# Kernel tuning notes

Measured on AMD Instinct MI355X. Metric: run time of the kernel, lower is better.

The kernel has to match this reference:

```python
import jax, jax.numpy as jnp
import numpy as np

FEAT_STRIDE = 16
PRE_NMS_TOP_N = 4000
POST_NMS_TOP_N = 300
NMS_THRESH = 0.7


def _whctrs(a):
    w = a[2] - a[0] + 1.0
    h = a[3] - a[1] + 1.0
    return w, h, a[0] + 0.5 * (w - 1.0), a[1] + 0.5 * (h - 1.0)

def _mkanchors(ws, hs, xc, yc):
    ws = ws[:, None]; hs = hs[:, None]
    return np.hstack([xc - 0.5 * (ws - 1), yc - 0.5 * (hs - 1), xc + 0.5 * (ws - 1), yc + 0.5 * (hs - 1)])

def _ratio_enum(anchor, ratios):
    w, h, xc, yc = _whctrs(anchor)
    size = w * h
    ws = np.round(np.sqrt(size / ratios))
    hs = np.round(ws * ratios)
    return _mkanchors(ws, hs, xc, yc)

def _scale_enum(anchor, scales):
    w, h, xc, yc = _whctrs(anchor)
    return _mkanchors(w * scales, h * scales, xc, yc)

def generate_anchors(base_size, ratios, scales):
    base = np.array([1.0, 1.0, base_size, base_size], dtype=np.float64) - 1.0
    ra = _ratio_enum(base, np.asarray(ratios, dtype=np.float64))
    return np.vstack([_scale_enum(ra[i], np.asarray(scales, dtype=np.float64)) for i in range(ra.shape[0])]).astype(np.float32)

# ---- NMS: sequential greedy suppression over score-sorted boxes ----

def _nms_keep(boxes, thresh):
    # boxes: [N,4] sorted by descending score. Legacy +1 area convention.
    boxes = jax.lax.stop_gradient(boxes)
    x1, y1, x2, y2 = boxes[:, 0], boxes[:, 1], boxes[:, 2], boxes[:, 3]
    areas = (x2 - x1 + 1.0) * (y2 - y1 + 1.0)
    xx1 = jnp.maximum(x1[:, None], x1[None, :])
    yy1 = jnp.maximum(y1[:, None], y1[None, :])
    xx2 = jnp.minimum(x2[:, None], x2[None, :])
    yy2 = jnp.minimum(y2[:, None], y2[None, :])
    w = jnp.maximum(xx2 - xx1 + 1.0, 0.0)
    h = jnp.maximum(yy2 - yy1 + 1.0, 0.0)
    inter = w * h
    iou = inter / (areas[:, None] + areas[None, :] - inter)
    sup = iou > thresh  # [N,N]
    n = boxes.shape[0]
    idxs = jnp.arange(n)

    def body(suppressed, i):
        kept = ~suppressed[i]
        suppressed = suppressed | (kept & sup[i] & (idxs > i))
        return suppressed, kept

    _, keep = jax.lax.scan(body, jnp.zeros((n,), dtype=bool), idxs)
    return keep  # [N] bool

# ---- forward ----

def _forward(scores, bbox_deltas, im_info, anchors):
    A = anchors.shape[0]
    B = bbox_deltas.shape[0]
    H, W = scores.shape[2], scores.shape[3]
    sc = scores[:, A:, :, :]  # fg scores [B,A,H,W]

    # anchor grid: K = H*W shifts, anchors broadcast over shifts (K major, A minor)
    shift_x = jnp.arange(W, dtype=scores.dtype) * FEAT_STRIDE
    shift_y = jnp.arange(H, dtype=scores.dtype) * FEAT_STRIDE
    sx, sy = jnp.meshgrid(shift_x, shift_y)  # 'xy' indexing, like np.meshgrid
    shifts = jnp.stack([sx.ravel(), sy.ravel(), sx.ravel(), sy.ravel()], axis=1)  # [K,4]
    all_anchors = (anchors[None, :, :] + shifts[:, None, :]).reshape(-1, 4)  # [K*A,4]

    deltas = bbox_deltas.transpose(0, 2, 3, 1).reshape(B, -1, 4)  # [B,N,4]
    scr = sc.transpose(0, 2, 3, 1).reshape(B, -1)  # [B,N]

    # bbox_transform_inv
    widths = all_anchors[:, 2] - all_anchors[:, 0] + 1.0
    heights = all_anchors[:, 3] - all_anchors[:, 1] + 1.0
    ctr_x = all_anchors[:, 0] + 0.5 * widths
    ctr_y = all_anchors[:, 1] + 0.5 * heights
    dx, dy, dw, dh = deltas[..., 0], deltas[..., 1], deltas[..., 2], deltas[..., 3]
    pcx = dx * widths + ctr_x
    pcy = dy * heights + ctr_y
    pw = jnp.exp(dw) * widths
    ph = jnp.exp(dh) * heights
    px1 = pcx - 0.5 * pw
    py1 = pcy - 0.5 * ph
    px2 = pcx + 0.5 * pw
    py2 = pcy + 0.5 * ph

    # clip_boxes per image: x in [0, W_img-1], y in [0, H_img-1]
    wmax = im_info[:, 1:2] - 1.0  # [B,1]
    hmax = im_info[:, 0:1] - 1.0
    px1 = jnp.clip(px1, 0.0, wmax)
    px2 = jnp.clip(px2, 0.0, wmax)
    py1 = jnp.clip(py1, 0.0, hmax)
    py2 = jnp.clip(py2, 0.0, hmax)
    proposals = jnp.stack([px1, py1, px2, py2], axis=-1)  # [B,N,4]

    def per_image(props, s, b_idx):
        _, order = jax.lax.top_k(s, PRE_NMS_TOP_N)  # descending
        p = props[order]  # [PRE,4]
        keep = _nms_keep(p, NMS_THRESH)
        ranks = jnp.cumsum(keep.astype(jnp.int32)) - 1
        slot = jnp.where(keep & (ranks < POST_NMS_TOP_N), ranks, POST_NMS_TOP_N)
        boxes_out = jnp.zeros((POST_NMS_TOP_N + 1, 4), p.dtype).at[slot].set(p)[:POST_NMS_TOP_N]
        col0 = jnp.full((POST_NMS_TOP_N, 1), b_idx.astype(p.dtype))
        return jnp.concatenate([col0, boxes_out], axis=1)  # [POST,5]

    return jax.vmap(per_image)(proposals, scr, jnp.arange(B))


def setup_inputs() -> dict:
    key = jax.random.key(0)
    k1, k2 = jax.random.split(key)
    B, A, H, W = 2, 9, 50, 50
    scores = jax.random.normal(k1, (B, 2 * A, H, W), dtype=jnp.float32)
    bbox_deltas = jax.random.normal(k2, (B, 4 * A, H, W), dtype=jnp.float32) * 0.1
    im_info = jnp.tile(jnp.array([[800.0, 800.0, 1.0]], dtype=jnp.float32), (B, 1))
    anchors = jnp.asarray(generate_anchors(16, [0.5, 1.0, 2.0], [8, 16, 32]))
    return {"scores": scores, "bbox_deltas": bbox_deltas, "im_info": im_info, "anchors": anchors}


def reference(scores, bbox_deltas, im_info, anchors):
    return _forward(scores, bbox_deltas, im_info, anchors)
```

## Files before the change

kernel.cpp:

```cpp
#include <hip/hip_runtime.h>
#include <stdint.h>

#define NA 9
#define HH 50
#define WW 50
#define NPROP (HH*WW*NA)
#define PRE_NMS 4000
#define POST_NMS 300
#define NWORDS 63
#define ROWSTRIDE 64
#define MROWS 4032
#define SELN 8192
#define NMS_T 0.7f
#define FSTRIDE 16.0f

typedef unsigned long long ull;

__device__ __forceinline__ uint32_t f32_ord(float s) {
    uint32_t u = __float_as_uint(s);
    return (u & 0x80000000u) ? ~u : (u | 0x80000000u);
}

__global__ void decode_hist(const float* __restrict__ scores,
                            const float* __restrict__ deltas,
                            const float* __restrict__ im_info,
                            const float* __restrict__ anchors,
                            ull* __restrict__ keys,
                            float4* __restrict__ boxes4,
                            uint32_t* __restrict__ hist, int B) {
    int t = blockIdx.x * blockDim.x + threadIdx.x;
    if (t >= B * NPROP) return;
    int b = t / NPROP;
    int i = t % NPROP;

    int a   = i % NA;
    int pos = i / NA;
    int w   = pos % WW;
    int h   = pos / WW;

    float score = scores[((size_t)b*2*NA + NA + a)*(HH*WW) + pos];
    ull key = ((ull)f32_ord(score) << 32) | (ull)(0xFFFFFFFFu - (uint32_t)i);
    keys[t] = key;
    atomicAdd(&hist[((uint32_t)b << 16) | (uint32_t)(key >> 48)], 1u);

    float ax1 = anchors[a*4+0], ay1 = anchors[a*4+1];
    float ax2 = anchors[a*4+2], ay2 = anchors[a*4+3];
    float sx = (float)w * FSTRIDE, sy = (float)h * FSTRIDE;
    float x1 = ax1 + sx, y1 = ay1 + sy, x2 = ax2 + sx, y2 = ay2 + sy;
    float bw = x2 - x1 + 1.0f;
    float bh = y2 - y1 + 1.0f;
    float cx = x1 + 0.5f * bw;
    float cy = y1 + 0.5f * bh;

    const float* dp = deltas + (size_t)b*4*NA*(HH*WW);
    float dx = dp[(4*a+0)*(HH*WW)+pos];
    float dy = dp[(4*a+1)*(HH*WW)+pos];
    float dw = dp[(4*a+2)*(HH*WW)+pos];
    float dh = dp[(4*a+3)*(HH*WW)+pos];

    float pcx = dx * bw + cx;
    float pcy = dy * bh + cy;
    float pw  = expf(dw) * bw;
    float ph  = expf(dh) * bh;

    float wmax = im_info[b*3+1] - 1.0f;
    float hmax = im_info[b*3+0] - 1.0f;
    float px1 = fminf(fmaxf(pcx - 0.5f*pw, 0.0f), wmax);
    float py1 = fminf(fmaxf(pcy - 0.5f*ph, 0.0f), hmax);
    float px2 = fminf(fmaxf(pcx + 0.5f*pw, 0.0f), wmax);
    float py2 = fminf(fmaxf(pcy + 0.5f*ph, 0.0f), hmax);

    boxes4[t] = make_float4(px1, py1, px2, py2);
}

__global__ __launch_bounds__(1024) void compact_kernel(
        const ull* __restrict__ keys,
        const uint32_t* __restrict__ hist,
        ull* __restrict__ ckeys,
        int* __restrict__ mcount) {
    __shared__ int sA[1024], sB[1024];
    __shared__ int nfine[64];
    __shared__ int sSeg, aboveC, thr, lcount;
    int img = blockIdx.x, tid = threadIdx.x;
    const uint32_t* h = hist + ((uint32_t)img << 16);

    {
        const uint4* h4 = (const uint4*)h;
        uint32_t s = 0;
        #pragma unroll
        for (int u = 0; u < 16; ++u) {
            uint4 v = h4[(tid << 4) | u];
            s += v.x + v.y + v.z + v.w;
        }
        sA[tid] = (int)s;
    }
    __syncthreads();
    int* curp = sA; int* nxtp = sB;
    for (int d = 1; d < 1024; d <<= 1) {
        int v = curp[tid] + ((tid + d < 1024) ? curp[tid + d] : 0);
        nxtp[tid] = v;
        __syncthreads();
        int* tmp = curp; curp = nxtp; nxtp = tmp;
    }
    {
        int cftS  = curp[tid];
        int cftS1 = (tid < 1023) ? curp[tid + 1] : 0;
        if (cftS >= PRE_NMS && cftS1 < PRE_NMS) { sSeg = tid; aboveC = cftS1; }
    }
    __syncthreads();
    if (tid < 64) nfine[tid] = (int)h[(sSeg << 6) | tid];
    __syncthreads();
    if (tid == 0) {
        int cum = aboveC;
        int t = sSeg << 6;
        for (int w = 63; w >= 0; --w) {
            int nc = cum + nfine[w];
            if (nc >= PRE_NMS) { t = (sSeg << 6) | w; break; }
            cum = nc;
        }
        thr = t;
        lcount = 0;
    }
    __syncthreads();

    ull* ck = ckeys + (size_t)img * SELN;
    {
        const ull* kb = keys + (size_t)img * NPROP;
        int th = thr;
        for (int i = tid; i < NPROP; i += 1024) {
            ull key = kb[i];
            if ((int)(key >> 48) >= th) {
                int p = atomicAdd(&lcount, 1);
                if (p < SELN) ck[p] = key;
            }
        }
    }
    __syncthreads();
    int M = lcount; if (M > SELN) M = SELN;
    if (tid == 0) mcount[img] = M;
    for (int e = M + tid; e < SELN; e += 1024) ck[e] = 0ull;
}

__global__ __launch_bounds__(256) void rank_scatter(
        const ull* __restrict__ ckeys,
        const int* __restrict__ mcount,
        const float4* __restrict__ boxes4,
        float4* __restrict__ gboxes) {
    __shared__ ull lk[SELN];
    __shared__ int sM;
    int img = blockIdx.y, rb = blockIdx.x, tid = threadIdx.x;
    if (tid == 0) sM = mcount[img];
    __syncthreads();
    int M = sM;
    if (rb * 256 >= M) return;
    int Ms = (M + 255) & ~255;

    const ull* kb = ckeys + (size_t)img * SELN;
    for (int e = tid; e < Ms; e += 256) lk[e] = (e < M) ? kb[e] : 0ull;
    __syncthreads();

    int row = rb * 256 + tid;
    if (row >= M) return;
    ull my = lk[row];

    int rank = 0;
    #pragma unroll 8
    for (int e = 0; e < Ms; ++e) rank += (lk[e] > my) ? 1 : 0;

    if (rank < PRE_NMS) {
        uint32_t idx = 0xFFFFFFFFu - (uint32_t)(my & 0xFFFFFFFFull);
        gboxes[(size_t)img*PRE_NMS + rank] = boxes4[(size_t)img*NPROP + idx];
    }
}

__global__ __launch_bounds__(64) void mask_kernel(const float4* __restrict__ gboxes,
                                                  ull* __restrict__ mask) {
    int rb = blockIdx.x, cb = blockIdx.y, b = blockIdx.z;
    if (cb < rb) return;
    __shared__ float cx1[64], cy1[64], cx2[64], cy2[64], car[64];
    int tid = threadIdx.x;

    int j0 = cb*64 + tid;
    float4 cbx = (j0 < PRE_NMS) ? gboxes[(size_t)b*PRE_NMS + j0]
                                : make_float4(0.f,0.f,0.f,0.f);
    cx1[tid]=cbx.x; cy1[tid]=cbx.y; cx2[tid]=cbx.z; cy2[tid]=cbx.w;
    car[tid]=(cbx.z-cbx.x+1.0f)*(cbx.w-cbx.y+1.0f);
    __syncthreads();

    int i = rb*64 + tid;
    if (i >= PRE_NMS) return;
    float4 rbx = gboxes[(size_t)b*PRE_NMS + i];
    float ix1=rbx.x, iy1=rbx.y, ix2=rbx.z, iy2=rbx.w;
    float iarea=(ix2-ix1+1.0f)*(iy2-iy1+1.0f);

    const bool diag = (rb == cb);
    ull bits = 0;
    #pragma unroll 16
    for (int k = 0; k < 64; ++k) {
        float xx1 = fmaxf(ix1, cx1[k]);
        float yy1 = fmaxf(iy1, cy1[k]);
        float xx2 = fminf(ix2, cx2[k]);
        float yy2 = fminf(iy2, cy2[k]);
        float ww = fmaxf(xx2 - xx1 + 1.0f, 0.0f);
        float hh = fmaxf(yy2 - yy1 + 1.0f, 0.0f);
        float inter = ww * hh;
        float iou = inter / (iarea + car[k] - inter);
        bool cond = diag ? (tid > k) : ((cb*64 + k) < PRE_NMS);
        if (cond & (iou > NMS_T)) bits |= (1ull << k);
    }
    mask[(((size_t)b*MROWS + i) << 6) + cb] = bits;
}

__global__ __launch_bounds__(64) void scan_kernel(const ull* __restrict__ mask,
                                                  const float4* __restrict__ gboxes,
                                                  float* __restrict__ out) {
    __shared__ ull buf[2][64][ROWSTRIDE];
    __shared__ int keep_idx[POST_NMS];
    int b = blockIdx.x;
    int lane = threadIdx.x;
    const ull* mbase = mask + ((size_t)b * MROWS << 6);

    ull supp = 0;
    if (lane == NWORDS-1) supp = 0xFFFFFFFF00000000ull;
    if (lane >= NWORDS)   supp = ~0ull;
    int kept = 0;
    bool done = false;
    int cur = 0;

    {
        const ulonglong2* src = (const ulonglong2*)mbase;
        ulonglong2* d2 = (ulonglong2*)buf[0];
        #pragma unroll
        for (int m = 0; m < 32; ++m) d2[lane + (m << 6)] = src[lane + (m << 6)];
        __syncthreads();
    }

    for (int wi = 0; wi < NWORDS && !done; ++wi) {
        ulonglong2 pf[32];
        bool havepf = (wi + 1 < NWORDS);
        if (havepf) {
            const ulonglong2* src =
                (const ulonglong2*)(mbase + (((size_t)(wi+1) << 6) << 6));
            #pragma unroll
            for (int m = 0; m < 32; ++m) pf[m] = src[lane + (m << 6)];
        }

        ull tw = buf[cur][lane][wi];
        ull avail = ~__shfl(supp, wi);
        ull keptmask = 0;

        while (avail) {
            int c = __builtin_ctzll(avail);
            if (lane == 0) keep_idx[kept] = (wi << 6) + c;
            ++kept;
            keptmask |= (1ull << c);
            if (kept >= POST_NMS) { done = true; break; }
            ull roww = __ballot((int)((tw >> c) & 1ull));
            avail &= ~roww;
            avail &= avail - 1;
        }

        if (!done) {
            ull km = keptmask;
            while (km) {
                int c = __builtin_ctzll(km); km &= km - 1;
                ull r = (lane > wi && lane < NWORDS) ? buf[cur][c][lane] : 0ull;
                supp |= r;
            }
            if (havepf) {
                ulonglong2* d2 = (ulonglong2*)buf[cur ^ 1];
                #pragma unroll
                for (int m = 0; m < 32; ++m) d2[lane + (m << 6)] = pf[m];
                __syncthreads();
                cur ^= 1;
            }
        }
    }
    __syncthreads();

    for (int r = lane; r < POST_NMS; r += 64) {
        float4 bx = (r < kept) ? gboxes[(size_t)b*PRE_NMS + keep_idx[r]]
                               : make_float4(0.f,0.f,0.f,0.f);
        float* o = out + (size_t)(b*POST_NMS + r)*5;
        o[0]=(float)b; o[1]=bx.x; o[2]=bx.y; o[3]=bx.z; o[4]=bx.w;
    }
}

extern "C" void kernel_launch(void* const* d_in, const int* in_sizes, int n_in,
                              void* d_out, int out_size, void* d_ws, size_t ws_size,
                              hipStream_t stream) {
    (void)n_in; (void)out_size; (void)ws_size;
    const float* scores  = (const float*)d_in[0];
    const float* deltas  = (const float*)d_in[1];
    const float* im_info = (const float*)d_in[2];
    const float* anchors = (const float*)d_in[3];
    float* out = (float*)d_out;

    const int B = in_sizes[0] / (2*NA*HH*WW);

    float4* boxes4 = (float4*)d_ws;
    float4* gboxes = boxes4 + (size_t)B*NPROP;
    ull*    keys   = (ull*)(gboxes + (size_t)B*PRE_NMS);
    ull*    ckeys  = keys + (size_t)B*NPROP;
    ull*    mask   = ckeys + (size_t)B*SELN;
    uint32_t* hist = (uint32_t*)(mask + ((size_t)B*MROWS << 6));
    int*    mcount = (int*)(hist + (size_t)B*65536);

    hipMemsetAsync(hist, 0, (size_t)B*65536*sizeof(uint32_t), stream);
    decode_hist<<<(B*NPROP + 255)/256, 256, 0, stream>>>(scores, deltas, im_info,
                                                         anchors, keys, boxes4, hist, B);
    compact_kernel<<<B, 1024, 0, stream>>>(keys, hist, ckeys, mcount);
    dim3 rgrid(SELN/256, B);
    rank_scatter<<<rgrid, 256, 0, stream>>>(ckeys, mcount, boxes4, gboxes);
    dim3 mgrid(NWORDS, NWORDS, B);
    mask_kernel<<<mgrid, 64, 0, stream>>>(gboxes, mask);
    scan_kernel<<<B, 64, 0, stream>>>(mask, gboxes, out);
}
```

Baseline: 259.2 us.

## Fuse decode with compaction and restructure NMS scan with transposed tiles

Merges decode and histogram/compaction into one per-image kernel that uses a 4096-bin shared-memory histogram. This removes the 512KB memset, the global atomics and the key buffer round trip, but it runs decode on only B blocks and reads the scores twice. The mask kernel also writes transposed diagonal and superdiagonal tiles. The scan kernel keeps those tiles in LDS and applies a cross-block correction via ballot, so it gathers only the kept rows from global memory instead of double-buffering 32KB of the mask per word. This targets the serial scan's per-word global load and barrier cost, at the price of lower parallelism in decode.

```diff
diff --git a/kernel.cpp b/kernel.cpp
--- a/kernel.cpp
+++ b/kernel.cpp
@@ -8,7 +8,6 @@
 #define PRE_NMS 4000
 #define POST_NMS 300
 #define NWORDS 63
-#define ROWSTRIDE 64
 #define MROWS 4032
 #define SELN 8192
 #define NMS_T 0.7f
@@ -21,78 +20,64 @@
     return (u & 0x80000000u) ? ~u : (u | 0x80000000u);
 }
 
-__global__ void decode_hist(const float* __restrict__ scores,
-                            const float* __restrict__ deltas,
-                            const float* __restrict__ im_info,
-                            const float* __restrict__ anchors,
-                            ull* __restrict__ keys,
-                            float4* __restrict__ boxes4,
-                            uint32_t* __restrict__ hist, int B) {
-    int t = blockIdx.x * blockDim.x + threadIdx.x;
-    if (t >= B * NPROP) return;
-    int b = t / NPROP;
-    int i = t % NPROP;
-
-    int a   = i % NA;
-    int pos = i / NA;
-    int w   = pos % WW;
-    int h   = pos / WW;
-
-    float score = scores[((size_t)b*2*NA + NA + a)*(HH*WW) + pos];
-    ull key = ((ull)f32_ord(score) << 32) | (ull)(0xFFFFFFFFu - (uint32_t)i);
-    keys[t] = key;
-    atomicAdd(&hist[((uint32_t)b << 16) | (uint32_t)(key >> 48)], 1u);
-
-    float ax1 = anchors[a*4+0], ay1 = anchors[a*4+1];
-    float ax2 = anchors[a*4+2], ay2 = anchors[a*4+3];
-    float sx = (float)w * FSTRIDE, sy = (float)h * FSTRIDE;
-    float x1 = ax1 + sx, y1 = ay1 + sy, x2 = ax2 + sx, y2 = ay2 + sy;
-    float bw = x2 - x1 + 1.0f;
-    float bh = y2 - y1 + 1.0f;
-    float cx = x1 + 0.5f * bw;
-    float cy = y1 + 0.5f * bh;
-
-    const float* dp = deltas + (size_t)b*4*NA*(HH*WW);
-    float dx = dp[(4*a+0)*(HH*WW)+pos];
-    float dy = dp[(4*a+1)*(HH*WW)+pos];
-    float dw = dp[(4*a+2)*(HH*WW)+pos];
-    float dh = dp[(4*a+3)*(HH*WW)+pos];
-
-    float pcx = dx * bw + cx;
-    float pcy = dy * bh + cy;
-    float pw  = expf(dw) * bw;
-    float ph  = expf(dh) * bh;
-
-    float wmax = im_info[b*3+1] - 1.0f;
-    float hmax = im_info[b*3+0] - 1.0f;
-    float px1 = fminf(fmaxf(pcx - 0.5f*pw, 0.0f), wmax);
-    float py1 = fminf(fmaxf(pcy - 0.5f*ph, 0.0f), hmax);
-    float px2 = fminf(fmaxf(pcx + 0.5f*pw, 0.0f), wmax);
-    float py2 = fminf(fmaxf(pcy + 0.5f*ph, 0.0f), hmax);
-
-    boxes4[t] = make_float4(px1, py1, px2, py2);
-}
-
-__global__ __launch_bounds__(1024) void compact_kernel(
-        const ull* __restrict__ keys,
-        const uint32_t* __restrict__ hist,
+__global__ __launch_bounds__(1024) void decode_compact(
+        const float* __restrict__ scores,
+        const float* __restrict__ deltas,
+        const float* __restrict__ im_info,
+        const float* __restrict__ anchors,
+        float4* __restrict__ boxes4,
         ull* __restrict__ ckeys,
         int* __restrict__ mcount) {
+    __shared__ int hist[4096];
     __shared__ int sA[1024], sB[1024];
-    __shared__ int nfine[64];
     __shared__ int sSeg, aboveC, thr, lcount;
     int img = blockIdx.x, tid = threadIdx.x;
-    const uint32_t* h = hist + ((uint32_t)img << 16);
+    for (int e = tid; e < 4096; e += 1024) hist[e] = 0;
+    float wmax = im_info[img*3+1] - 1.0f;
+    float hmax = im_info[img*3+0] - 1.0f;
+    __syncthreads();
+
+    for (int i = tid; i < NPROP; i += 1024) {
+        int a   = i % NA;
+        int pos = i / NA;
+        int w   = pos % WW;
+        int h   = pos / WW;
+
+        float score = scores[((size_t)img*2*NA + NA + a)*(HH*WW) + pos];
+        atomicAdd(&hist[f32_ord(score) >> 20], 1);
+
+        float ax1 = anchors[a*4+0], ay1 = anchors[a*4+1];
+        float ax2 = anchors[a*4+2], ay2 = anchors[a*4+3];
+        float sx = (float)w * FSTRIDE, sy = (float)h * FSTRIDE;
+        float x1 = ax1 + sx, y1 = ay1 + sy, x2 = ax2 + sx, y2 = ay2 + sy;
+        float bw = x2 - x1 + 1.0f;
+        float bh = y2 - y1 + 1.0f;
+        float cx = x1 + 0.5f * bw;
+        float cy = y1 + 0.5f * bh;
+
+        const float* dp = deltas + (size_t)img*4*NA*(HH*WW);
+        float dx = dp[(4*a+0)*(HH*WW)+pos];
+        float dy = dp[(4*a+1)*(HH*WW)+pos];
+        float dw = dp[(4*a+2)*(HH*WW)+pos];
+        float dh = dp[(4*a+3)*(HH*WW)+pos];
+
+        float pcx = dx * bw + cx;
+        float pcy = dy * bh + cy;
+        float pw  = expf(dw) * bw;
+        float ph  = expf(dh) * bh;
+
+        float px1 = fminf(fmaxf(pcx - 0.5f*pw, 0.0f), wmax);
+        float py1 = fminf(fmaxf(pcy - 0.5f*ph, 0.0f), hmax);
+        float px2 = fminf(fmaxf(pcx + 0.5f*pw, 0.0f), wmax);
+        float py2 = fminf(fmaxf(pcy + 0.5f*ph, 0.0f), hmax);
+
+        boxes4[(size_t)img*NPROP + i] = make_float4(px1, py1, px2, py2);
+    }
+    __syncthreads();
 
     {
-        const uint4* h4 = (const uint4*)h;
-        uint32_t s = 0;
-        #pragma unroll
-        for (int u = 0; u < 16; ++u) {
-            uint4 v = h4[(tid << 4) | u];
-            s += v.x + v.y + v.z + v.w;
-        }
-        sA[tid] = (int)s;
+        int t4 = tid << 2;
+        sA[tid] = hist[t4] + hist[t4+1] + hist[t4+2] + hist[t4+3];
     }
     __syncthreads();
     int* curp = sA; int* nxtp = sB;
@@ -103,35 +88,32 @@
         int* tmp = curp; curp = nxtp; nxtp = tmp;
     }
     {
-        int cftS  = curp[tid];
-        int cftS1 = (tid < 1023) ? curp[tid + 1] : 0;
-        if (cftS >= PRE_NMS && cftS1 < PRE_NMS) { sSeg = tid; aboveC = cftS1; }
-    }
-    __syncthreads();
-    if (tid < 64) nfine[tid] = (int)h[(sSeg << 6) | tid];
+        int c0 = curp[tid];
+        int c1 = (tid < 1023) ? curp[tid + 1] : 0;
+        if (c0 >= PRE_NMS && c1 < PRE_NMS) { sSeg = tid; aboveC = c1; }
+    }
     __syncthreads();
     if (tid == 0) {
-        int cum = aboveC;
-        int t = sSeg << 6;
-        for (int w = 63; w >= 0; --w) {
-            int nc = cum + nfine[w];
-            if (nc >= PRE_NMS) { t = (sSeg << 6) | w; break; }
+        int cum = aboveC, t = sSeg << 2;
+        for (int w = 3; w >= 0; --w) {
+            int nc = cum + hist[(sSeg << 2) + w];
+            if (nc >= PRE_NMS) { t = (sSeg << 2) + w; break; }
             cum = nc;
         }
-        thr = t;
-        lcount = 0;
+        thr = t; lcount = 0;
     }
     __syncthreads();
 
     ull* ck = ckeys + (size_t)img * SELN;
     {
-        const ull* kb = keys + (size_t)img * NPROP;
         int th = thr;
         for (int i = tid; i < NPROP; i += 1024) {
-            ull key = kb[i];
-            if ((int)(key >> 48) >= th) {
+            int a = i % NA, pos = i / NA;
+            float score = scores[((size_t)img*2*NA + NA + a)*(HH*WW) + pos];
+            uint32_t so = f32_ord(score);
+            if ((int)(so >> 20) >= th) {
                 int p = atomicAdd(&lcount, 1);
-                if (p < SELN) ck[p] = key;
+                if (p < SELN) ck[p] = ((ull)so << 32) | (ull)(0xFFFFFFFFu - (uint32_t)i);
             }
         }
     }
@@ -174,10 +156,13 @@
 }
 
 __global__ __launch_bounds__(64) void mask_kernel(const float4* __restrict__ gboxes,
-                                                  ull* __restrict__ mask) {
+                                                  ull* __restrict__ mask,
+                                                  ull* __restrict__ diagT,
+                                                  ull* __restrict__ superT) {
     int rb = blockIdx.x, cb = blockIdx.y, b = blockIdx.z;
     if (cb < rb) return;
     __shared__ float cx1[64], cy1[64], cx2[64], cy2[64], car[64];
+    __shared__ float rx1[64], ry1[64], rx2[64], ry2[64], rar[64];
     int tid = threadIdx.x;
 
     int j0 = cb*64 + tid;
@@ -185,15 +170,39 @@
                                 : make_float4(0.f,0.f,0.f,0.f);
     cx1[tid]=cbx.x; cy1[tid]=cbx.y; cx2[tid]=cbx.z; cy2[tid]=cbx.w;
     car[tid]=(cbx.z-cbx.x+1.0f)*(cbx.w-cbx.y+1.0f);
-    __syncthreads();
 
     int i = rb*64 + tid;
-    if (i >= PRE_NMS) return;
-    float4 rbx = gboxes[(size_t)b*PRE_NMS + i];
-    float ix1=rbx.x, iy1=rbx.y, ix2=rbx.z, iy2=rbx.w;
-    float iarea=(ix2-ix1+1.0f)*(iy2-iy1+1.0f);
+    float4 rbx = (i < PRE_NMS) ? gboxes[(size_t)b*PRE_NMS + i]
+                               : make_float4(0.f,0.f,0.f,0.f);
+    rx1[tid]=rbx.x; ry1[tid]=rbx.y; rx2[tid]=rbx.z; ry2[tid]=rbx.w;
+    rar[tid]=(rbx.z-rbx.x+1.0f)*(rbx.w-rbx.y+1.0f);
+    __syncthreads();
+
+    if (cb == rb + 1) {
+        float mx1=cbx.x, my1=cbx.y, mx2=cbx.z, my2=cbx.w, marea=car[tid];
+        ull tb = 0;
+        #pragma unroll 16
+        for (int k = 0; k < 64; ++k) {
+            float xx1 = fmaxf(mx1, rx1[k]);
+            float yy1 = fmaxf(my1, ry1[k]);
+            float xx2 = fminf(mx2, rx2[k]);
+            float yy2 = fminf(my2, ry2[k]);
+            float ww = fmaxf(xx2 - xx1 + 1.0f, 0.0f);
+            float hh = fmaxf(yy2 - yy1 + 1.0f, 0.0f);
+            float inter = ww * hh;
+            float iou = inter / (marea + rar[k] - inter);
+            if (iou > NMS_T) tb |= (1ull << k);
+        }
+        superT[((size_t)b*(NWORDS-1) + rb)*64 + tid] = tb;
+    }
 
     const bool diag = (rb == cb);
+    if (i >= PRE_NMS) {
+        if (diag) diagT[((size_t)b*NWORDS + rb)*64 + tid] = 0ull;
+        return;
+    }
+    float ix1=rbx.x, iy1=rbx.y, ix2=rbx.z, iy2=rbx.w, iarea=rar[tid];
+
     ull bits = 0;
     #pragma unroll 16
     for (int k = 0; k < 64; ++k) {
@@ -209,44 +218,47 @@
         if (cond & (iou > NMS_T)) bits |= (1ull << k);
     }
     mask[(((size_t)b*MROWS + i) << 6) + cb] = bits;
+    if (diag) diagT[((size_t)b*NWORDS + rb)*64 + tid] = bits;
 }
 
 __global__ __launch_bounds__(64) void scan_kernel(const ull* __restrict__ mask,
+                                                  const ull* __restrict__ diagT,
+                                                  const ull* __restrict__ superT,
                                                   const float4* __restrict__ gboxes,
                                                   float* __restrict__ out) {
-    __shared__ ull buf[2][64][ROWSTRIDE];
+    __shared__ __align__(16) ull dTl[NWORDS*64];
+    __shared__ __align__(16) ull sTl[(NWORDS-1)*64];
     __shared__ int keep_idx[POST_NMS];
     int b = blockIdx.x;
     int lane = threadIdx.x;
-    const ull* mbase = mask + ((size_t)b * MROWS << 6);
-
+
+    {
+        const ulonglong2* gd = (const ulonglong2*)(diagT + (size_t)b*NWORDS*64);
+        ulonglong2* dd = (ulonglong2*)dTl;
+        for (int e = lane; e < NWORDS*32; e += 64) dd[e] = gd[e];
+        const ulonglong2* gs = (const ulonglong2*)(superT + (size_t)b*(NWORDS-1)*64);
+        ulonglong2* ds = (ulonglong2*)sTl;
+        for (int e = lane; e < (NWORDS-1)*32; e += 64) ds[e] = gs[e];
+    }
+    __syncthreads();
+
+    const ull* mrow = mask + ((size_t)b * MROWS << 6);
     ull supp = 0;
     if (lane == NWORDS-1) supp = 0xFFFFFFFF00000000ull;
     if (lane >= NWORDS)   supp = ~0ull;
     int kept = 0;
     bool done = false;
-    int cur = 0;
-
-    {
-        const ulonglong2* src = (const ulonglong2*)mbase;
-        ulonglong2* d2 = (ulonglong2*)buf[0];
-        #pragma unroll
-        for (int m = 0; m < 32; ++m) d2[lane + (m << 6)] = src[lane + (m << 6)];
-        __syncthreads();
-    }
-
+    ull corr = 0;
+    ull pend = 0;
+
+    ull tw = dTl[lane];
     for (int wi = 0; wi < NWORDS && !done; ++wi) {
-        ulonglong2 pf[32];
-        bool havepf = (wi + 1 < NWORDS);
-        if (havepf) {
-            const ulonglong2* src =
-                (const ulonglong2*)(mbase + (((size_t)(wi+1) << 6) << 6));
-            #pragma unroll
-            for (int m = 0; m < 32; ++m) pf[m] = src[lane + (m << 6)];
-        }
-
-        ull tw = buf[cur][lane][wi];
-        ull avail = ~__shfl(supp, wi);
+        ull twn = (wi + 1 < NWORDS) ? dTl[(wi+1)*64 + lane] : 0ull;
+        ull tw2 = (wi + 1 < NWORDS) ? sTl[wi*64 + lane]     : 0ull;
+
+        ull cur = __shfl(supp, wi) | corr;
+        supp |= pend; pend = 0;
+        ull avail = ~cur;
         ull keptmask = 0;
 
         while (avail) {
@@ -261,20 +273,35 @@
         }
 
         if (!done) {
+            corr = __ballot((int)((tw2 & keptmask) != 0ull));
+            const bool ld = (lane > wi) && (lane < NWORDS);
+            const ull* base = mrow + ((size_t)wi << 12) + lane;
             ull km = keptmask;
             while (km) {
-                int c = __builtin_ctzll(km); km &= km - 1;
-                ull r = (lane > wi && lane < NWORDS) ? buf[cur][c][lane] : 0ull;
-                supp |= r;
+                int c0 = __builtin_ctzll(km); km &= km - 1;
+                int c1 = -1, c2 = -1, c3 = -1, c4 = -1, c5 = -1, c6 = -1, c7 = -1;
+                if (km) { c1 = __builtin_ctzll(km); km &= km - 1; }
+                if (km) { c2 = __builtin_ctzll(km); km &= km - 1; }
+                if (km) { c3 = __builtin_ctzll(km); km &= km - 1; }
+                if (km) { c4 = __builtin_ctzll(km); km &= km - 1; }
+                if (km) { c5 = __builtin_ctzll(km); km &= km - 1; }
+                if (km) { c6 = __builtin_ctzll(km); km &= km - 1; }
+                if (km) { c7 = __builtin_ctzll(km); km &= km - 1; }
+                ull v0=0,v1=0,v2=0,v3=0,v4=0,v5=0,v6=0,v7=0;
+                if (ld) {
+                    v0 = base[(size_t)c0 << 6];
+                    if (c1 >= 0) v1 = base[(size_t)c1 << 6];
+                    if (c2 >= 0) v2 = base[(size_t)c2 << 6];
+                    if (c3 >= 0) v3 = base[(size_t)c3 << 6];
+                    if (c4 >= 0) v4 = base[(size_t)c4 << 6];
+                    if (c5 >= 0) v5 = base[(size_t)c5 << 6];
+                    if (c6 >= 0) v6 = base[(size_t)c6 << 6];
+                    if (c7 >= 0) v7 = base[(size_t)c7 << 6];
+                }
+                pend |= (v0 | v1 | v2 | v3) | (v4 | v5 | v6 | v7);
             }
-            if (havepf) {
-                ulonglong2* d2 = (ulonglong2*)buf[cur ^ 1];
-                #pragma unroll
-                for (int m = 0; m < 32; ++m) d2[lane + (m << 6)] = pf[m];
-                __syncthreads();
-                cur ^= 1;
-            }
-        }
+        }
+        tw = twn;
     }
     __syncthreads();
 
@@ -300,19 +327,17 @@
 
     float4* boxes4 = (float4*)d_ws;
     float4* gboxes = boxes4 + (size_t)B*NPROP;
-    ull*    keys   = (ull*)(gboxes + (size_t)B*PRE_NMS);
-    ull*    ckeys  = keys + (size_t)B*NPROP;
+    ull*    ckeys  = (ull*)(gboxes + (size_t)B*PRE_NMS);
     ull*    mask   = ckeys + (size_t)B*SELN;
-    uint32_t* hist = (uint32_t*)(mask + ((size_t)B*MROWS << 6));
-    int*    mcount = (int*)(hist + (size_t)B*65536);
-
-    hipMemsetAsync(hist, 0, (size_t)B*65536*sizeof(uint32_t), stream);
-    decode_hist<<<(B*NPROP + 255)/256, 256, 0, stream>>>(scores, deltas, im_info,
-                                                         anchors, keys, boxes4, hist, B);
-    compact_kernel<<<B, 1024, 0, stream>>>(keys, hist, ckeys, mcount);
+    ull*    diagT  = mask + ((size_t)B*MROWS << 6);
+    ull*    superT = diagT + (size_t)B*NWORDS*64;
+    int*    mcount = (int*)(superT + (size_t)B*(NWORDS-1)*64);
+
+    decode_compact<<<B, 1024, 0, stream>>>(scores, deltas, im_info, anchors,
+                                           boxes4, ckeys, mcount);
     dim3 rgrid(SELN/256, B);
     rank_scatter<<<rgrid, 256, 0, stream>>>(ckeys, mcount, boxes4, gboxes);
     dim3 mgrid(NWORDS, NWORDS, B);
-    mask_kernel<<<mgrid, 64, 0, stream>>>(gboxes, mask);
-    scan_kernel<<<B, 64, 0, stream>>>(mask, gboxes, out);
-}
+    mask_kernel<<<mgrid, 64, 0, stream>>>(gboxes, mask, diagT, superT);
+    scan_kernel<<<B, 64, 0, stream>>>(mask, diagT, superT, gboxes, out);
+}
```

Measured after the change: 303.5 us. +17.1%, slower.

## Fuse proposal pipeline into one persistent kernel with grid barriers

Applied to the files above, without the earlier changes.

Merges decode, threshold selection, compaction, ranking, IoU mask and greedy scan into a single persistent kernel of 256 blocks, using atomic-counter grid barriers between phases in place of separate launches. It also shrinks the histogram to 4096 bins per image, so the threshold search and memset get smaller, and switches compaction to wave-aggregated atomics spread across all blocks. The goal is to cut per-launch overhead and the serial single-block compaction. The cost is spin-wait barriers, which depend on all 256 blocks being co-resident. The final scan now runs with 256 threads where only one wave does the greedy work, which adds a block-wide sync every word.

```diff
diff --git a/kernel.cpp b/kernel.cpp
--- a/kernel.cpp
+++ b/kernel.cpp
@@ -8,11 +8,12 @@
 #define PRE_NMS 4000
 #define POST_NMS 300
 #define NWORDS 63
-#define ROWSTRIDE 64
 #define MROWS 4032
 #define SELN 8192
 #define NMS_T 0.7f
 #define FSTRIDE 16.0f
+#define NBLK 256
+#define NTHR 256
 
 typedef unsigned long long ull;
 
@@ -21,268 +22,301 @@
     return (u & 0x80000000u) ? ~u : (u | 0x80000000u);
 }
 
-__global__ void decode_hist(const float* __restrict__ scores,
-                            const float* __restrict__ deltas,
-                            const float* __restrict__ im_info,
-                            const float* __restrict__ anchors,
-                            ull* __restrict__ keys,
-                            float4* __restrict__ boxes4,
-                            uint32_t* __restrict__ hist, int B) {
-    int t = blockIdx.x * blockDim.x + threadIdx.x;
-    if (t >= B * NPROP) return;
-    int b = t / NPROP;
-    int i = t % NPROP;
-
-    int a   = i % NA;
-    int pos = i / NA;
-    int w   = pos % WW;
-    int h   = pos / WW;
-
-    float score = scores[((size_t)b*2*NA + NA + a)*(HH*WW) + pos];
-    ull key = ((ull)f32_ord(score) << 32) | (ull)(0xFFFFFFFFu - (uint32_t)i);
-    keys[t] = key;
-    atomicAdd(&hist[((uint32_t)b << 16) | (uint32_t)(key >> 48)], 1u);
-
-    float ax1 = anchors[a*4+0], ay1 = anchors[a*4+1];
-    float ax2 = anchors[a*4+2], ay2 = anchors[a*4+3];
-    float sx = (float)w * FSTRIDE, sy = (float)h * FSTRIDE;
-    float x1 = ax1 + sx, y1 = ay1 + sy, x2 = ax2 + sx, y2 = ay2 + sy;
-    float bw = x2 - x1 + 1.0f;
-    float bh = y2 - y1 + 1.0f;
-    float cx = x1 + 0.5f * bw;
-    float cy = y1 + 0.5f * bh;
-
-    const float* dp = deltas + (size_t)b*4*NA*(HH*WW);
-    float dx = dp[(4*a+0)*(HH*WW)+pos];
-    float dy = dp[(4*a+1)*(HH*WW)+pos];
-    float dw = dp[(4*a+2)*(HH*WW)+pos];
-    float dh = dp[(4*a+3)*(HH*WW)+pos];
-
-    float pcx = dx * bw + cx;
-    float pcy = dy * bh + cy;
-    float pw  = expf(dw) * bw;
-    float ph  = expf(dh) * bh;
-
-    float wmax = im_info[b*3+1] - 1.0f;
-    float hmax = im_info[b*3+0] - 1.0f;
-    float px1 = fminf(fmaxf(pcx - 0.5f*pw, 0.0f), wmax);
-    float py1 = fminf(fmaxf(pcy - 0.5f*ph, 0.0f), hmax);
-    float px2 = fminf(fmaxf(pcx + 0.5f*pw, 0.0f), wmax);
-    float py2 = fminf(fmaxf(pcy + 0.5f*ph, 0.0f), hmax);
-
-    boxes4[t] = make_float4(px1, py1, px2, py2);
+__device__ __forceinline__ void gbar(int* bar, int k) {
+    __threadfence();
+    __syncthreads();
+    if (threadIdx.x == 0) {
+        atomicAdd(&bar[k], 1);
+        while (atomicAdd(&bar[k], 0) < NBLK) __builtin_amdgcn_s_sleep(8);
+    }
+    __syncthreads();
+    __threadfence();
 }
 
-__global__ __launch_bounds__(1024) void compact_kernel(
-        const ull* __restrict__ keys,
-        const uint32_t* __restrict__ hist,
+__global__ __launch_bounds__(NTHR) void proposal_all(
+        const float* __restrict__ scores,
+        const float* __restrict__ deltas,
+        const float* __restrict__ im_info,
+        const float* __restrict__ anchors,
+        uint32_t* __restrict__ hist,
+        int* __restrict__ cnt,
+        int* __restrict__ bar,
+        float4* __restrict__ boxes4,
+        ull* __restrict__ keys,
         ull* __restrict__ ckeys,
-        int* __restrict__ mcount) {
-    __shared__ int sA[1024], sB[1024];
-    __shared__ int nfine[64];
-    __shared__ int sSeg, aboveC, thr, lcount;
-    int img = blockIdx.x, tid = threadIdx.x;
-    const uint32_t* h = hist + ((uint32_t)img << 16);
+        float4* __restrict__ gboxes,
+        ull* __restrict__ mask,
+        float* __restrict__ out, int B) {
+    __shared__ __align__(16) char pool[65536];
+    __shared__ int sA[NTHR], sB[NTHR];
+    __shared__ int sThr[8];
+    __shared__ int keepIdx[POST_NMS];
+    __shared__ int sKept, sDone;
+
+    const int bid = blockIdx.x, tid = threadIdx.x;
+    const int lane = tid & 63, wid = tid >> 6;
+
+    for (int i0 = bid * NTHR; i0 < B * NPROP; i0 += NBLK * NTHR) {
+        int t = i0 + tid;
+        if (t < B * NPROP) {
+            int img = t / NPROP;
+            int i   = t - img * NPROP;
+            int a   = i % NA;
+            int pos = i / NA;
+            int w   = pos % WW;
+            int h   = pos / WW;
+
+            float score = scores[((size_t)img*2*NA + NA + a)*(HH*WW) + pos];
+            uint32_t so = f32_ord(score);
+            keys[t] = ((ull)so << 32) | (ull)(0xFFFFFFFFu - (uint32_t)i);
+            atomicAdd(&hist[((uint32_t)img << 12) | (so >> 20)], 1u);
+
+            float ax1 = anchors[a*4+0], ay1 = anchors[a*4+1];
+            float ax2 = anchors[a*4+2], ay2 = anchors[a*4+3];
+            float sx = (float)w * FSTRIDE, sy = (float)h * FSTRIDE;
+            float x1 = ax1 + sx, y1 = ay1 + sy, x2 = ax2 + sx, y2 = ay2 + sy;
+            float bw = x2 - x1 + 1.0f;
+            float bh = y2 - y1 + 1.0f;
+            float cx = x1 + 0.5f * bw;
+            float cy = y1 + 0.5f * bh;
+
+            const float* dp = deltas + (size_t)img*4*NA*(HH*WW);
+            float dx = dp[(4*a+0)*(HH*WW)+pos];
+            float dy = dp[(4*a+1)*(HH*WW)+pos];
+            float dw = dp[(4*a+2)*(HH*WW)+pos];
+            float dh = dp[(4*a+3)*(HH*WW)+pos];
+
+            float pcx = dx * bw + cx;
+            float pcy = dy * bh + cy;
+            float pw  = expf(dw) * bw;
+            float ph  = expf(dh) * bh;
+
+            float wmax = im_info[img*3+1] - 1.0f;
+            float hmax = im_info[img*3+0] - 1.0f;
+            float px1 = fminf(fmaxf(pcx - 0.5f*pw, 0.0f), wmax);
+            float py1 = fminf(fmaxf(pcy - 0.5f*ph, 0.0f), hmax);
+            float px2 = fminf(fmaxf(pcx + 0.5f*pw, 0.0f), wmax);
+            float py2 = fminf(fmaxf(pcy + 0.5f*ph, 0.0f), hmax);
+
+            boxes4[t] = make_float4(px1, py1, px2, py2);
+        }
+    }
+    gbar(bar, 0);
+
+    for (int img = 0; img < B; ++img) {
+        const uint32_t* h = hist + ((uint32_t)img << 12);
+        {
+            const uint4* h4 = (const uint4*)h;
+            uint32_t s = 0;
+            #pragma unroll
+            for (int u = 0; u < 4; ++u) {
+                uint4 v = h4[(tid << 2) | u];
+                s += v.x + v.y + v.z + v.w;
+            }
+            sA[tid] = (int)s;
+        }
+        __syncthreads();
+        int* curp = sA; int* nxtp = sB;
+        for (int d = 1; d < NTHR; d <<= 1) {
+            int v = curp[tid] + ((tid + d < NTHR) ? curp[tid + d] : 0);
+            nxtp[tid] = v;
+            __syncthreads();
+            int* tmp = curp; curp = nxtp; nxtp = tmp;
+        }
+        {
+            int c0 = curp[tid];
+            int c1 = (tid < NTHR-1) ? curp[tid + 1] : 0;
+            if (c0 >= PRE_NMS && c1 < PRE_NMS) {
+                int cum = c1, t = tid << 4;
+                for (int w = 15; w >= 0; --w) {
+                    int nc = cum + (int)h[(tid << 4) + w];
+                    if (nc >= PRE_NMS) { t = (tid << 4) + w; break; }
+                    cum = nc;
+                }
+                sThr[img] = t;
+            }
+        }
+        __syncthreads();
+    }
+    for (int img = 0; img < B; ++img) {
+        int th = sThr[img];
+        const ull* kb = keys + (size_t)img * NPROP;
+        ull* ck = ckeys + (size_t)img * SELN;
+        for (int i0 = bid * NTHR; i0 < NPROP; i0 += NBLK * NTHR) {
+            int i = i0 + tid;
+            ull key = 0; bool q = false;
+            if (i < NPROP) { key = kb[i]; q = ((int)(key >> 52) >= th); }
+            ull ball = __ballot(q);
+            if (ball) {
+                int leader = __builtin_ctzll(ball);
+                int nb = __popcll(ball);
+                int basep = 0;
+                if (lane == leader) basep = atomicAdd(&cnt[img], nb);
+                basep = __shfl(basep, leader);
+                if (q) {
+                    int p = basep + __popcll(ball & ((1ull << lane) - 1ull));
+                    if (p < SELN) ck[p] = key;
+                }
+            }
+        }
+    }
+    gbar(bar, 1);
+
+    if (bid < B * 32) {
+        int img = bid >> 5, tile = bid & 31;
+        int M = cnt[img]; if (M > SELN) M = SELN;
+        if (tile * NTHR < M) {
+            ull* lk = (ull*)pool;
+            int Ms = (M + NTHR - 1) & ~(NTHR - 1);
+            const ull* kb = ckeys + (size_t)img * SELN;
+            for (int e = tid; e < Ms; e += NTHR) lk[e] = (e < M) ? kb[e] : 0ull;
+            __syncthreads();
+            int row = tile * NTHR + tid;
+            if (row < M) {
+                ull my = lk[row];
+                int rank = 0;
+                #pragma unroll 8
+                for (int e = 0; e < Ms; ++e) rank += (lk[e] > my) ? 1 : 0;
+                if (rank < PRE_NMS) {
+                    uint32_t idx = 0xFFFFFFFFu - (uint32_t)(my & 0xFFFFFFFFull);
+                    gboxes[(size_t)img*PRE_NMS + rank] = boxes4[(size_t)img*NPROP + idx];
+                }
+            }
+        }
+    }
+    gbar(bar, 2);
 
     {
-        const uint4* h4 = (const uint4*)h;
-        uint32_t s = 0;
-        #pragma unroll
-        for (int u = 0; u < 16; ++u) {
-            uint4 v = h4[(tid << 4) | u];
-            s += v.x + v.y + v.z + v.w;
-        }
-        sA[tid] = (int)s;
-    }
-    __syncthreads();
-    int* curp = sA; int* nxtp = sB;
-    for (int d = 1; d < 1024; d <<= 1) {
-        int v = curp[tid] + ((tid + d < 1024) ? curp[tid + d] : 0);
-        nxtp[tid] = v;
+        float* st = (float*)(pool + wid * 1536);
+        float* scx1 = st;        float* scy1 = st + 64;
+        float* scx2 = st + 128;  float* scy2 = st + 192;
+        float* scar = st + 256;
+        const int npairs = NWORDS * (NWORDS + 1) / 2;
+        const int total = B * npairs;
+        const int slots = NBLK * 4;
+        const int trips = (total + slots - 1) / slots;
+        for (int it = 0; it < trips; ++it) {
+            int pid = it * slots + bid * 4 + wid;
+            bool act = pid < total;
+            int b = 0, rb = 0, cb = 0;
+            if (act) {
+                b = pid / npairs;
+                int rem = pid - b * npairs;
+                while (rem >= NWORDS - rb) { rem -= NWORDS - rb; ++rb; }
+                cb = rb + rem;
+            }
+            if (act) {
+                int j0 = cb * 64 + lane;
+                float4 cbx = (j0 < PRE_NMS) ? gboxes[(size_t)b*PRE_NMS + j0]
+                                            : make_float4(0.f, 0.f, 0.f, 0.f);
+                scx1[lane] = cbx.x; scy1[lane] = cbx.y;
+                scx2[lane] = cbx.z; scy2[lane] = cbx.w;
+                scar[lane] = (cbx.z - cbx.x + 1.0f) * (cbx.w - cbx.y + 1.0f);
+            }
+            __syncthreads();
+            if (act) {
+                int i = rb * 64 + lane;
+                if (i < PRE_NMS) {
+                    float4 rbx = gboxes[(size_t)b*PRE_NMS + i];
+                    float ix1 = rbx.x, iy1 = rbx.y, ix2 = rbx.z, iy2 = rbx.w;
+                    float iarea = (ix2 - ix1 + 1.0f) * (iy2 - iy1 + 1.0f);
+                    const bool diag = (rb == cb);
+                    ull bits = 0;
+                    #pragma unroll 16
+                    for (int k = 0; k < 64; ++k) {
+                        float xx1 = fmaxf(ix1, scx1[k]);
+                        float yy1 = fmaxf(iy1, scy1[k]);
+                        float xx2 = fminf(ix2, scx2[k]);
+                        float yy2 = fminf(iy2, scy2[k]);
+                        float ww = fmaxf(xx2 - xx1 + 1.0f, 0.0f);
+                        float hh = fmaxf(yy2 - yy1 + 1.0f, 0.0f);
+                        float inter = ww * hh;
+                        float iou = inter / (iarea + scar[k] - inter);
+                        bool cond = diag ? (lane > k) : ((cb * 64 + k) < PRE_NMS);
+                        if (cond & (iou > NMS_T)) bits |= (1ull << k);
+                    }
+                    mask[(((size_t)b*MROWS + i) << 6) + cb] = bits;
+                }
+            }
+            __syncthreads();
+        }
+    }
+    gbar(bar, 3);
+
+    if (bid < B) {
+        int b = bid;
+        ull* buf0 = (ull*)pool;
+        ull* buf1 = (ull*)pool + 4096;
+        const ull* mbase = mask + ((size_t)b * MROWS << 6);
+
+        {
+            const ulonglong2* src = (const ulonglong2*)mbase;
+            ulonglong2* dst = (ulonglong2*)buf0;
+            #pragma unroll
+            for (int k = 0; k < 8; ++k) dst[tid + k*NTHR] = src[tid + k*NTHR];
+        }
+        if (tid == 0) { sDone = 0; sKept = 0; }
         __syncthreads();
-        int* tmp = curp; curp = nxtp; nxtp = tmp;
-    }
-    {
-        int cftS  = curp[tid];
-        int cftS1 = (tid < 1023) ? curp[tid + 1] : 0;
-        if (cftS >= PRE_NMS && cftS1 < PRE_NMS) { sSeg = tid; aboveC = cftS1; }
-    }
-    __syncthreads();
-    if (tid < 64) nfine[tid] = (int)h[(sSeg << 6) | tid];
-    __syncthreads();
-    if (tid == 0) {
-        int cum = aboveC;
-        int t = sSeg << 6;
-        for (int w = 63; w >= 0; --w) {
-            int nc = cum + nfine[w];
-            if (nc >= PRE_NMS) { t = (sSeg << 6) | w; break; }
-            cum = nc;
-        }
-        thr = t;
-        lcount = 0;
-    }
-    __syncthreads();
-
-    ull* ck = ckeys + (size_t)img * SELN;
-    {
-        const ull* kb = keys + (size_t)img * NPROP;
-        int th = thr;
-        for (int i = tid; i < NPROP; i += 1024) {
-            ull key = kb[i];
-            if ((int)(key >> 48) >= th) {
-                int p = atomicAdd(&lcount, 1);
-                if (p < SELN) ck[p] = key;
-            }
-        }
-    }
-    __syncthreads();
-    int M = lcount; if (M > SELN) M = SELN;
-    if (tid == 0) mcount[img] = M;
-    for (int e = M + tid; e < SELN; e += 1024) ck[e] = 0ull;
-}
-
-__global__ __launch_bounds__(256) void rank_scatter(
-        const ull* __restrict__ ckeys,
-        const int* __restrict__ mcount,
-        const float4* __restrict__ boxes4,
-        float4* __restrict__ gboxes) {
-    __shared__ ull lk[SELN];
-    __shared__ int sM;
-    int img = blockIdx.y, rb = blockIdx.x, tid = threadIdx.x;
-    if (tid == 0) sM = mcount[img];
-    __syncthreads();
-    int M = sM;
-    if (rb * 256 >= M) return;
-    int Ms = (M + 255) & ~255;
-
-    const ull* kb = ckeys + (size_t)img * SELN;
-    for (int e = tid; e < Ms; e += 256) lk[e] = (e < M) ? kb[e] : 0ull;
-    __syncthreads();
-
-    int row = rb * 256 + tid;
-    if (row >= M) return;
-    ull my = lk[row];
-
-    int rank = 0;
-    #pragma unroll 8
-    for (int e = 0; e < Ms; ++e) rank += (lk[e] > my) ? 1 : 0;
-
-    if (rank < PRE_NMS) {
-        uint32_t idx = 0xFFFFFFFFu - (uint32_t)(my & 0xFFFFFFFFull);
-        gboxes[(size_t)img*PRE_NMS + rank] = boxes4[(size_t)img*NPROP + idx];
-    }
-}
-
-__global__ __launch_bounds__(64) void mask_kernel(const float4* __restrict__ gboxes,
-                                                  ull* __restrict__ mask) {
-    int rb = blockIdx.x, cb = blockIdx.y, b = blockIdx.z;
-    if (cb < rb) return;
-    __shared__ float cx1[64], cy1[64], cx2[64], cy2[64], car[64];
-    int tid = threadIdx.x;
-
-    int j0 = cb*64 + tid;
-    float4 cbx = (j0 < PRE_NMS) ? gboxes[(size_t)b*PRE_NMS + j0]
-                                : make_float4(0.f,0.f,0.f,0.f);
-    cx1[tid]=cbx.x; cy1[tid]=cbx.y; cx2[tid]=cbx.z; cy2[tid]=cbx.w;
-    car[tid]=(cbx.z-cbx.x+1.0f)*(cbx.w-cbx.y+1.0f);
-    __syncthreads();
-
-    int i = rb*64 + tid;
-    if (i >= PRE_NMS) return;
-    float4 rbx = gboxes[(size_t)b*PRE_NMS + i];
-    float ix1=rbx.x, iy1=rbx.y, ix2=rbx.z, iy2=rbx.w;
-    float iarea=(ix2-ix1+1.0f)*(iy2-iy1+1.0f);
-
-    const bool diag = (rb == cb);
-    ull bits = 0;
-    #pragma unroll 16
-    for (int k = 0; k < 64; ++k) {
-        float xx1 = fmaxf(ix1, cx1[k]);
-        float yy1 = fmaxf(iy1, cy1[k]);
-        float xx2 = fminf(ix2, cx2[k]);
-        float yy2 = fminf(iy2, cy2[k]);
-        float ww = fmaxf(xx2 - xx1 + 1.0f, 0.0f);
-        float hh = fmaxf(yy2 - yy1 + 1.0f, 0.0f);
-        float inter = ww * hh;
-        float iou = inter / (iarea + car[k] - inter);
-        bool cond = diag ? (tid > k) : ((cb*64 + k) < PRE_NMS);
-        if (cond & (iou > NMS_T)) bits |= (1ull << k);
-    }
-    mask[(((size_t)b*MROWS + i) << 6) + cb] = bits;
-}
-
-__global__ __launch_bounds__(64) void scan_kernel(const ull* __restrict__ mask,
-                                                  const float4* __restrict__ gboxes,
-                                                  float* __restrict__ out) {
-    __shared__ ull buf[2][64][ROWSTRIDE];
-    __shared__ int keep_idx[POST_NMS];
-    int b = blockIdx.x;
-    int lane = threadIdx.x;
-    const ull* mbase = mask + ((size_t)b * MROWS << 6);
-
-    ull supp = 0;
-    if (lane == NWORDS-1) supp = 0xFFFFFFFF00000000ull;
-    if (lane >= NWORDS)   supp = ~0ull;
-    int kept = 0;
-    bool done = false;
-    int cur = 0;
-
-    {
-        const ulonglong2* src = (const ulonglong2*)mbase;
-        ulonglong2* d2 = (ulonglong2*)buf[0];
-        #pragma unroll
-        for (int m = 0; m < 32; ++m) d2[lane + (m << 6)] = src[lane + (m << 6)];
+
+        ull supp = 0;
+        if (lane == NWORDS-1) supp = 0xFFFFFFFF00000000ull;
+        if (lane >= NWORDS)   supp = ~0ull;
+        int kept = 0;
+        int cur = 0;
+
+        for (int wi = 0; wi < NWORDS; ++wi) {
+            ulonglong2 pf[8];
+            bool havepf = (wi + 1 < NWORDS);
+            if (havepf) {
+                const ulonglong2* src =
+                    (const ulonglong2*)(mbase + ((size_t)(wi + 1) << 12));
+                #pragma unroll
+                for (int k = 0; k < 8; ++k) pf[k] = src[tid + k*NTHR];
+            }
+            if (wid == 0) {
+                ull* bc = cur ? buf1 : buf0;
+                ull tw = bc[lane * 64 + wi];
+                ull avail = ~__shfl(supp, wi);
+                ull keptmask = 0;
+                bool done = false;
+                while (avail) {
+                    int c = __builtin_ctzll(avail);
+                    if (lane == 0) keepIdx[kept] = (wi << 6) + c;
+                    ++kept;
+                    keptmask |= (1ull << c);
+                    if (kept >= POST_NMS) { done = true; break; }
+                    ull roww = __ballot((int)((tw >> c) & 1ull));
+                    avail &= ~roww;
+                    avail &= avail - 1;
+                }
+                if (!done) {
+                    ull km = keptmask;
+                    while (km) {
+                        int c = __builtin_ctzll(km); km &= km - 1;
+                        ull r = (lane > wi && lane < NWORDS) ? bc[c * 64 + lane] : 0ull;
+                        supp |= r;
+                    }
+                }
+                if (lane == 0) { sKept = kept; sDone = done ? 1 : 0; }
+            }
+            __syncthreads();
+            if (sDone) break;
+            if (havepf) {
+                ulonglong2* dst = (ulonglong2*)(cur ? buf0 : buf1);
+                #pragma unroll
+                for (int k = 0; k < 8; ++k) dst[tid + k*NTHR] = pf[k];
+            }
+            __syncthreads();
+            cur ^= 1;
+        }
         __syncthreads();
-    }
-
-    for (int wi = 0; wi < NWORDS && !done; ++wi) {
-        ulonglong2 pf[32];
-        bool havepf = (wi + 1 < NWORDS);
-        if (havepf) {
-            const ulonglong2* src =
-                (const ulonglong2*)(mbase + (((size_t)(wi+1) << 6) << 6));
-            #pragma unroll
-            for (int m = 0; m < 32; ++m) pf[m] = src[lane + (m << 6)];
-        }
-
-        ull tw = buf[cur][lane][wi];
-        ull avail = ~__shfl(supp, wi);
-        ull keptmask = 0;
-
-        while (avail) {
-            int c = __builtin_ctzll(avail);
-            if (lane == 0) keep_idx[kept] = (wi << 6) + c;
-            ++kept;
-            keptmask |= (1ull << c);
-            if (kept >= POST_NMS) { done = true; break; }
-            ull roww = __ballot((int)((tw >> c) & 1ull));
-            avail &= ~roww;
-            avail &= avail - 1;
-        }
-
-        if (!done) {
-            ull km = keptmask;
-            while (km) {
-                int c = __builtin_ctzll(km); km &= km - 1;
-                ull r = (lane > wi && lane < NWORDS) ? buf[cur][c][lane] : 0ull;
-                supp |= r;
-            }
-            if (havepf) {
-                ulonglong2* d2 = (ulonglong2*)buf[cur ^ 1];
-                #pragma unroll
-                for (int m = 0; m < 32; ++m) d2[lane + (m << 6)] = pf[m];
-                __syncthreads();
-                cur ^= 1;
-            }
-        }
-    }
-    __syncthreads();
-
-    for (int r = lane; r < POST_NMS; r += 64) {
-        float4 bx = (r < kept) ? gboxes[(size_t)b*PRE_NMS + keep_idx[r]]
-                               : make_float4(0.f,0.f,0.f,0.f);
-        float* o = out + (size_t)(b*POST_NMS + r)*5;
-        o[0]=(float)b; o[1]=bx.x; o[2]=bx.y; o[3]=bx.z; o[4]=bx.w;
+        int kfin = sKept;
+        for (int r = tid; r < POST_NMS; r += NTHR) {
+            float4 bx = (r < kfin) ? gboxes[(size_t)b*PRE_NMS + keepIdx[r]]
+                                   : make_float4(0.f, 0.f, 0.f, 0.f);
+            float* o = out + (size_t)(b*POST_NMS + r)*5;
+            o[0] = (float)b; o[1] = bx.x; o[2] = bx.y; o[3] = bx.z; o[4] = bx.w;
+        }
     }
 }
 
@@ -298,21 +332,19 @@
 
     const int B = in_sizes[0] / (2*NA*HH*WW);
 
-    float4* boxes4 = (float4*)d_ws;
-    float4* gboxes = boxes4 + (size_t)B*NPROP;
-    ull*    keys   = (ull*)(gboxes + (size_t)B*PRE_NMS);
-    ull*    ckeys  = keys + (size_t)B*NPROP;
-    ull*    mask   = ckeys + (size_t)B*SELN;
-    uint32_t* hist = (uint32_t*)(mask + ((size_t)B*MROWS << 6));
-    int*    mcount = (int*)(hist + (size_t)B*65536);
-
-    hipMemsetAsync(hist, 0, (size_t)B*65536*sizeof(uint32_t), stream);
-    decode_hist<<<(B*NPROP + 255)/256, 256, 0, stream>>>(scores, deltas, im_info,
-                                                         anchors, keys, boxes4, hist, B);
-    compact_kernel<<<B, 1024, 0, stream>>>(keys, hist, ckeys, mcount);
-    dim3 rgrid(SELN/256, B);
-    rank_scatter<<<rgrid, 256, 0, stream>>>(ckeys, mcount, boxes4, gboxes);
-    dim3 mgrid(NWORDS, NWORDS, B);
-    mask_kernel<<<mgrid, 64, 0, stream>>>(gboxes, mask);
-    scan_kernel<<<B, 64, 0, stream>>>(mask, gboxes, out);
+    size_t histB = (size_t)B * 4096 * sizeof(uint32_t);
+    uint32_t* hist = (uint32_t*)d_ws;
+    int* cnt = (int*)((char*)d_ws + histB);
+    int* bar = cnt + 8;
+    float4* boxes4 = (float4*)((char*)d_ws + histB + 64);
+    ull* keys  = (ull*)(boxes4 + (size_t)B*NPROP);
+    ull* ckeys = keys + (size_t)B*NPROP;
+    float4* gboxes = (float4*)(ckeys + (size_t)B*SELN);
+    ull* mask = (ull*)(gboxes + (size_t)B*PRE_NMS);
+
+    hipMemsetAsync(d_ws, 0, histB + 64, stream);
+    proposal_all<<<NBLK, NTHR, 0, stream>>>(scores, deltas, im_info, anchors,
+                                            hist, cnt, bar,
+                                            boxes4, keys, ckeys, gboxes, mask,
+                                            out, B);
 }
```

After: 417.5 us. 61.1% more time.
